# Kernel optimization log

Measured on AMD Instinct MI355X. Metric: run time of the kernel, lower is better.

The kernel has to match this reference:

```python
import jax, jax.numpy as jnp
import numpy as np
from jax import lax

B, S, H, E, TOP_K = 4, 2048, 8192, 256, 8

def setup_inputs() -> dict:
    key = jax.random.key(0)
    kx, kw = jax.random.split(key)
    x = jax.random.normal(kx, (B, S, H), dtype=jnp.float32)
    # Dense kernel init scale ~ 1/sqrt(H)
    W_router = jax.random.normal(kw, (H, E), dtype=jnp.float32) * (1.0 / np.sqrt(H))
    return {"x": x, "W_router": W_router}

def reference(x, W_router):
    # router_logits: [B, S, E]
    router_logits = jnp.einsum('bsh,he->bse', x, W_router)
    top_logits, top_indices = lax.top_k(router_logits, k=TOP_K)  # [B,S,K]
    routing_weights = jax.nn.softmax(top_logits, axis=-1)        # [B,S,K]
    return routing_weights, top_indices, router_logits
```

## Files before the change

### kernel.cpp

```cpp
#include <hip/hip_runtime.h>
#include <math.h>
#include <float.h>

typedef _Float16 half8 __attribute__((ext_vector_type(8)));
typedef float f32x4 __attribute__((ext_vector_type(4)));

namespace {
constexpr int kH = 8192, kE = 256, kTopK = 8, kTok = 8192;
constexpr int kIdxOff = kTok * kTopK;
constexpr int kLogitsOff = 2 * kTok * kTopK;
constexpr int kBM = 128, kBN = 128, kBK = 32;
constexpr int kPadH = 40;
constexpr int kCand = 16;
constexpr float kEps = 5e-5f;
constexpr float kInvScale = 1.0f / 262144.0f;
constexpr size_t kWtF   = (size_t)kE * kH;
constexpr size_t kWtlF  = kWtF + (size_t)kE * kH / 2;
constexpr size_t kPartF = kWtF + (size_t)kE * kH;
constexpr size_t kPartStride = (size_t)kTok * kE;
}

__global__ __launch_bounds__(1024)
void prep_w(const float* __restrict__ W, float* __restrict__ Wt,
            _Float16* __restrict__ Wth, _Float16* __restrict__ Wtl) {
    __shared__ float tile[32][33];
    const int k0 = blockIdx.x * 32, e0 = blockIdx.y * 32;
    const int tx = threadIdx.x, ty = threadIdx.y;
    tile[ty][tx] = W[(size_t)(k0 + ty) * kE + (e0 + tx)];
    __syncthreads();
    const float v = tile[tx][ty];
    const size_t o = (size_t)(e0 + ty) * kH + (k0 + tx);
    Wt[o] = v;
    const float vs = v * 256.0f;
    const _Float16 h = (_Float16)vs;
    Wth[o] = h;
    Wtl[o] = (_Float16)(vs - (float)h);
}

__global__ __launch_bounds__(256, 2)
void router_gemm_mfma(const float* __restrict__ x,
                      const _Float16* __restrict__ Wth,
                      const _Float16* __restrict__ Wtl,
                      float* __restrict__ p0, float* __restrict__ pws,
                      int kchunk)
{
    __shared__ _Float16 sxh[kBM][kPadH], sxl[kBM][kPadH];
    __shared__ _Float16 swh[kBN][kPadH], swl[kBN][kPadH];

    const int tid  = threadIdx.x;
    const int lane = tid & 63;
    const int w    = tid >> 6;
    const int wm   = w >> 1, wn = w & 1;
    const int t0   = blockIdx.x * kBM;
    const int e0   = blockIdx.y * kBN;
    const int kc   = blockIdx.z;
    const int kbase = kc * kchunk;
    const int nsteps = kchunk / kBK;

    f32x4 acc[4][4];
    #pragma unroll
    for (int m = 0; m < 4; ++m)
        #pragma unroll
        for (int n = 0; n < 4; ++n) {
            acc[m][n][0] = 0.f; acc[m][n][1] = 0.f;
            acc[m][n][2] = 0.f; acc[m][n][3] = 0.f;
        }

    const int srow = tid >> 1;
    const int scg  = (tid & 1) << 4;
    const float*    xp  = x   + (size_t)(t0 + srow) * kH + kbase + scg;
    const _Float16* whp = Wth + (size_t)(e0 + srow) * kH + kbase + scg;
    const _Float16* wlp = Wtl + (size_t)(e0 + srow) * kH + kbase + scg;

    float4 xv0, xv1, xv2, xv3;
    uint4  wh0, wh1, wl0, wl1;
    {
        xv0 = *reinterpret_cast<const float4*>(xp);
        xv1 = *reinterpret_cast<const float4*>(xp + 4);
        xv2 = *reinterpret_cast<const float4*>(xp + 8);
        xv3 = *reinterpret_cast<const float4*>(xp + 12);
        wh0 = *reinterpret_cast<const uint4*>(whp);
        wh1 = *reinterpret_cast<const uint4*>(whp + 8);
        wl0 = *reinterpret_cast<const uint4*>(wlp);
        wl1 = *reinterpret_cast<const uint4*>(wlp + 8);
    }

    const int fr = lane & 15;
    const int fk = (lane >> 4) << 3;

    for (int t = 0; t < nsteps; ++t) {
        float xf[16];
        xf[0]=xv0.x; xf[1]=xv0.y; xf[2]=xv0.z; xf[3]=xv0.w;
        xf[4]=xv1.x; xf[5]=xv1.y; xf[6]=xv1.z; xf[7]=xv1.w;
        xf[8]=xv2.x; xf[9]=xv2.y; xf[10]=xv2.z; xf[11]=xv2.w;
        xf[12]=xv3.x; xf[13]=xv3.y; xf[14]=xv3.z; xf[15]=xv3.w;
        half8 h0, h1, l0, l1;
        #pragma unroll
        for (int i = 0; i < 8; ++i) {
            const float sA = xf[i] * 1024.0f;
            const _Float16 hA = (_Float16)sA;
            h0[i] = hA; l0[i] = (_Float16)(sA - (float)hA);
            const float sB = xf[i + 8] * 1024.0f;
            const _Float16 hB = (_Float16)sB;
            h1[i] = hB; l1[i] = (_Float16)(sB - (float)hB);
        }
        *reinterpret_cast<half8*>(&sxh[srow][scg])     = h0;
        *reinterpret_cast<half8*>(&sxh[srow][scg + 8]) = h1;
        *reinterpret_cast<half8*>(&sxl[srow][scg])     = l0;
        *reinterpret_cast<half8*>(&sxl[srow][scg + 8]) = l1;
        *reinterpret_cast<uint4*>(&swh[srow][scg])     = wh0;
        *reinterpret_cast<uint4*>(&swh[srow][scg + 8]) = wh1;
        *reinterpret_cast<uint4*>(&swl[srow][scg])     = wl0;
        *reinterpret_cast<uint4*>(&swl[srow][scg + 8]) = wl1;
        __syncthreads();

        if (t + 1 < nsteps) {
            const size_t o = (size_t)(t + 1) * kBK;
            xv0 = *reinterpret_cast<const float4*>(xp + o);
            xv1 = *reinterpret_cast<const float4*>(xp + o + 4);
            xv2 = *reinterpret_cast<const float4*>(xp + o + 8);
            xv3 = *reinterpret_cast<const float4*>(xp + o + 12);
            wh0 = *reinterpret_cast<const uint4*>(whp + o);
            wh1 = *reinterpret_cast<const uint4*>(whp + o + 8);
            wl0 = *reinterpret_cast<const uint4*>(wlp + o);
            wl1 = *reinterpret_cast<const uint4*>(wlp + o + 8);
        }

        half8 ah[4], al[4];
        #pragma unroll
        for (int m = 0; m < 4; ++m) {
            ah[m] = *reinterpret_cast<const half8*>(&sxh[(wm << 6) + (m << 4) + fr][fk]);
            al[m] = *reinterpret_cast<const half8*>(&sxl[(wm << 6) + (m << 4) + fr][fk]);
        }
        #pragma unroll
        for (int n = 0; n < 4; ++n) {
            const half8 bh = *reinterpret_cast<const half8*>(&swh[(wn << 6) + (n << 4) + fr][fk]);
            const half8 bl = *reinterpret_cast<const half8*>(&swl[(wn << 6) + (n << 4) + fr][fk]);
            #pragma unroll
            for (int m = 0; m < 4; ++m) {
                acc[m][n] = __builtin_amdgcn_mfma_f32_16x16x32_f16(ah[m], bh, acc[m][n], 0, 0, 0);
                acc[m][n] = __builtin_amdgcn_mfma_f32_16x16x32_f16(ah[m], bl, acc[m][n], 0, 0, 0);
                acc[m][n] = __builtin_amdgcn_mfma_f32_16x16x32_f16(al[m], bh, acc[m][n], 0, 0, 0);
            }
        }
        __syncthreads();
    }

    float* dst = (kc == 0) ? p0 : (pws + (size_t)(kc - 1) * kPartStride);
    const int r0 = (lane >> 4) << 2;
    const int c0 = lane & 15;
    #pragma unroll
    for (int m = 0; m < 4; ++m)
        #pragma unroll
        for (int n = 0; n < 4; ++n) {
            const int col = e0 + (wn << 6) + (n << 4) + c0;
            #pragma unroll
            for (int r = 0; r < 4; ++r) {
                const int row = t0 + (wm << 6) + (m << 4) + r0 + r;
                dst[(size_t)row * kE + col] = acc[m][n][r] * kInvScale;
            }
        }
}

#define ARGMAX_ROUND(r)                                                        \
    {                                                                          \
        float bv = v0; int bi = (lane << 2);                                   \
        if (v1 > bv) { bv = v1; bi = (lane << 2) + 1; }                        \
        if (v2 > bv) { bv = v2; bi = (lane << 2) + 2; }                        \
        if (v3 > bv) { bv = v3; bi = (lane << 2) + 3; }                        \
        _Pragma("unroll")                                                      \
        for (int off = 32; off > 0; off >>= 1) {                               \
            const float ov = __shfl_xor(bv, off, 64);                          \
            const int   oi = __shfl_xor(bi, off, 64);                          \
            if (ov > bv || (ov == bv && oi < bi)) { bv = ov; bi = oi; }        \
        }                                                                      \
        if (lane == (r)) { myv = bv; myi = bi; }                               \
        if ((bi >> 2) == lane) {                                               \
            const int m = bi & 3;                                              \
            if      (m == 0) v0 = -FLT_MAX;                                    \
            else if (m == 1) v1 = -FLT_MAX;                                    \
            else if (m == 2) v2 = -FLT_MAX;                                    \
            else             v3 = -FLT_MAX;                                    \
        }                                                                      \
    }

__global__ __launch_bounds__(256)
void combine_select(const float* __restrict__ x, const float* __restrict__ Wt,
                    const float* __restrict__ pws, float* __restrict__ out,
                    int npart)
{
    const int lane = threadIdx.x & 63;
    const int w    = threadIdx.x >> 6;
    const int row  = blockIdx.x * 4 + w;
    float* logits = out + kLogitsOff;
    const size_t rb = (size_t)row * kE + (lane << 2);

    float4 s = *reinterpret_cast<const float4*>(logits + rb);
    for (int p = 0; p < npart; ++p) {
        const float4 q = *reinterpret_cast<const float4*>(pws + (size_t)p * kPartStride + rb);
        s.x += q.x; s.y += q.y; s.z += q.z; s.w += q.w;
    }
    *reinterpret_cast<float4*>(logits + rb) = s;

    float v0 = s.x, v1 = s.y, v2 = s.z, v3 = s.w;
    float myv = -FLT_MAX; int myi = -1;

    #pragma unroll
    for (int r = 0; r < 9; ++r) ARGMAX_ROUND(r)

    const float nv = __shfl_down(myv, 1, 64);
    const unsigned long long amb = __ballot(lane < 8 && (myv - nv) < kEps);

    if (amb == 0ull) {
        const float m = __shfl(myv, 0, 64);
        const float e = (lane < kTopK) ? expf(myv - m) : 0.f;
        float t = e;
        #pragma unroll
        for (int off = 1; off < 8; off <<= 1) t += __shfl_xor(t, off, 64);
        if (lane < kTopK) {
            out[(size_t)row * kTopK + lane]           = e / t;
            out[kIdxOff + (size_t)row * kTopK + lane] = (float)myi;
        }
    } else {
        #pragma unroll
        for (int r = 9; r < kCand; ++r) ARGMAX_ROUND(r)

        const float* xr = x + (size_t)row * kH;
        double dv = -1.0e300;
        #pragma unroll 1
        for (int cg = 0; cg < kCand; cg += 4) {
            const int i0 = __shfl(myi, cg + 0, 64);
            const int i1 = __shfl(myi, cg + 1, 64);
            const int i2 = __shfl(myi, cg + 2, 64);
            const int i3 = __shfl(myi, cg + 3, 64);
            const float* w0 = Wt + (size_t)i0 * kH;
            const float* w1 = Wt + (size_t)i1 * kH;
            const float* w2 = Wt + (size_t)i2 * kH;
            const float* w3 = Wt + (size_t)i3 * kH;
            double a0 = 0.0, a1 = 0.0, a2 = 0.0, a3 = 0.0;
            for (int k = (lane << 2); k < kH; k += 256) {
                const float4 xv = *reinterpret_cast<const float4*>(xr + k);
                const float4 q0 = *reinterpret_cast<const float4*>(w0 + k);
                const float4 q1 = *reinterpret_cast<const float4*>(w1 + k);
                const float4 q2 = *reinterpret_cast<const float4*>(w2 + k);
                const float4 q3 = *reinterpret_cast<const float4*>(w3 + k);
                a0 = fma((double)xv.x, (double)q0.x, a0);
                a1 = fma((double)xv.x, (double)q1.x, a1);
                a2 = fma((double)xv.x, (double)q2.x, a2);
                a3 = fma((double)xv.x, (double)q3.x, a3);
                a0 = fma((double)xv.y, (double)q0.y, a0);
                a1 = fma((double)xv.y, (double)q1.y, a1);
                a2 = fma((double)xv.y, (double)q2.y, a2);
                a3 = fma((double)xv.y, (double)q3.y, a3);
                a0 = fma((double)xv.z, (double)q0.z, a0);
                a1 = fma((double)xv.z, (double)q1.z, a1);
                a2 = fma((double)xv.z, (double)q2.z, a2);
                a3 = fma((double)xv.z, (double)q3.z, a3);
                a0 = fma((double)xv.w, (double)q0.w, a0);
                a1 = fma((double)xv.w, (double)q1.w, a1);
                a2 = fma((double)xv.w, (double)q2.w, a2);
                a3 = fma((double)xv.w, (double)q3.w, a3);
            }
            #pragma unroll
            for (int off = 32; off > 0; off >>= 1) {
                a0 += __shfl_xor(a0, off, 64);
                a1 += __shfl_xor(a1, off, 64);
                a2 += __shfl_xor(a2, off, 64);
                a3 += __shfl_xor(a3, off, 64);
            }
            if (lane == cg + 0) dv = a0;
            if (lane == cg + 1) dv = a1;
            if (lane == cg + 2) dv = a2;
            if (lane == cg + 3) dv = a3;
        }

        double cv = dv; int ci = myi;
        double mx = 0.0, ssum = 0.0, keepv = 0.0; int keepi = 0;
        #pragma unroll 1
        for (int r = 0; r < kTopK; ++r) {
            double bv = cv; int bi = ci;
            #pragma unroll
            for (int off = 32; off > 0; off >>= 1) {
                const double ov = __shfl_xor(bv, off, 64);
                const int    oi = __shfl_xor(bi, off, 64);
                if (ov > bv || (ov == bv && oi < bi)) { bv = ov; bi = oi; }
            }
            if (r == 0) mx = bv;
            ssum += exp(bv - mx);
            if (lane == r) { keepv = bv; keepi = bi; }
            if (ci == bi) cv = -1.0e300;
        }
        if (lane < kTopK) {
            out[(size_t)row * kTopK + lane]           = (float)(exp(keepv - mx) / ssum);
            out[kIdxOff + (size_t)row * kTopK + lane] = (float)keepi;
        }
    }
}

extern "C" void kernel_launch(void* const* d_in, const int* in_sizes, int n_in,
                              void* d_out, int out_size, void* d_ws, size_t ws_size,
                              hipStream_t stream) {
    const float* x  = (const float*)d_in[0];
    const float* Wr = (const float*)d_in[1];
    float* out = (float*)d_out;
    float* Wt  = (float*)d_ws;
    _Float16* Wth = (_Float16*)((float*)d_ws + kWtF);
    _Float16* Wtl = (_Float16*)((float*)d_ws + kWtlF);
    float* pws = (float*)d_ws + kPartF;
    (void)in_sizes; (void)n_in; (void)out_size;

    const size_t need4 = (kPartF + 3 * kPartStride) * sizeof(float);
    const int nkc = (ws_size >= need4) ? 4 : 2;
    const int kchunk = kH / nkc;

    hipLaunchKernelGGL(prep_w, dim3(kH / 32, kE / 32), dim3(32, 32), 0, stream,
                       Wr, Wt, Wth, Wtl);
    hipLaunchKernelGGL(router_gemm_mfma, dim3(kTok / kBM, kE / kBN, nkc), dim3(256),
                       0, stream, x, Wth, Wtl, out + kLogitsOff, pws, kchunk);
    hipLaunchKernelGGL(combine_select, dim3(kTok / 4), dim3(256), 0, stream,
                       x, Wt, pws, out, nkc - 1);
}
```

Baseline: 215.4 us.

## Load weight tiles directly into LDS with swizzled layout and raise split-K

Weight hi/lo fp16 tiles are now loaded with global_load_lds, going straight from global memory to LDS and skipping registers. The prep kernel writes them in an XOR-swizzled k order so the unpadded LDS tile avoids bank conflicts on MFMA operand reads. The split-K count rises from 4 to 8 when the workspace allows, adding parallelism at the cost of more partial buffers for the combine kernel to read and reduce. The direct LDS writes happen in the same iteration as the compute, with no double buffering, so load latency may still be exposed.

```diff
diff --git a/kernel.cpp b/kernel.cpp
--- a/kernel.cpp
+++ b/kernel.cpp
@@ -20,6 +20,16 @@
 constexpr size_t kPartStride = (size_t)kTok * kE;
 }
 
+__device__ __forceinline__ void gld16(const _Float16* g, _Float16* l) {
+    __builtin_amdgcn_global_load_lds(
+        (const __attribute__((address_space(1))) void*)g,
+        (__attribute__((address_space(3))) void*)l, 16, 0, 0);
+}
+
+__device__ __forceinline__ int kswz(int e, int k) {
+    return (k & ~31) | (((((k >> 3) & 3) ^ ((e >> 1) & 3))) << 3) | (k & 7);
+}
+
 __global__ __launch_bounds__(1024)
 void prep_w(const float* __restrict__ W, float* __restrict__ Wt,
             _Float16* __restrict__ Wth, _Float16* __restrict__ Wtl) {
@@ -29,12 +39,13 @@
     tile[ty][tx] = W[(size_t)(k0 + ty) * kE + (e0 + tx)];
     __syncthreads();
     const float v = tile[tx][ty];
-    const size_t o = (size_t)(e0 + ty) * kH + (k0 + tx);
-    Wt[o] = v;
+    const int e = e0 + ty, k = k0 + tx;
+    Wt[(size_t)e * kH + k] = v;
     const float vs = v * 256.0f;
     const _Float16 h = (_Float16)vs;
-    Wth[o] = h;
-    Wtl[o] = (_Float16)(vs - (float)h);
+    const size_t os = (size_t)e * kH + kswz(e, k);
+    Wth[os] = h;
+    Wtl[os] = (_Float16)(vs - (float)h);
 }
 
 __global__ __launch_bounds__(256, 2)
@@ -44,8 +55,10 @@
                       float* __restrict__ p0, float* __restrict__ pws,
                       int kchunk)
 {
-    __shared__ _Float16 sxh[kBM][kPadH], sxl[kBM][kPadH];
-    __shared__ _Float16 swh[kBN][kPadH], swl[kBN][kPadH];
+    __shared__ __align__(16) _Float16 sxh[kBM * kPadH];
+    __shared__ __align__(16) _Float16 sxl[kBM * kPadH];
+    __shared__ __align__(16) _Float16 swh[kBN * kBK];
+    __shared__ __align__(16) _Float16 swl[kBN * kBK];
 
     const int tid  = threadIdx.x;
     const int lane = tid & 63;
@@ -53,8 +66,7 @@
     const int wm   = w >> 1, wn = w & 1;
     const int t0   = blockIdx.x * kBM;
     const int e0   = blockIdx.y * kBN;
-    const int kc   = blockIdx.z;
-    const int kbase = kc * kchunk;
+    const int kbase = blockIdx.z * kchunk;
     const int nsteps = kchunk / kBK;
 
     f32x4 acc[4][4];
@@ -66,29 +78,35 @@
             acc[m][n][2] = 0.f; acc[m][n][3] = 0.f;
         }
 
+    const size_t wro0 = (size_t)(e0 + (w << 4) + (lane >> 2)) * kH
+                        + kbase + ((lane & 3) << 3);
+    const size_t wro1 = wro0 + (size_t)64 * kH;
+    _Float16* lwh0 = swh + (w << 9);
+    _Float16* lwh1 = swh + (w << 9) + 2048;
+    _Float16* lwl0 = swl + (w << 9);
+    _Float16* lwl1 = swl + (w << 9) + 2048;
+
     const int srow = tid >> 1;
     const int scg  = (tid & 1) << 4;
-    const float*    xp  = x   + (size_t)(t0 + srow) * kH + kbase + scg;
-    const _Float16* whp = Wth + (size_t)(e0 + srow) * kH + kbase + scg;
-    const _Float16* wlp = Wtl + (size_t)(e0 + srow) * kH + kbase + scg;
-
-    float4 xv0, xv1, xv2, xv3;
-    uint4  wh0, wh1, wl0, wl1;
-    {
-        xv0 = *reinterpret_cast<const float4*>(xp);
-        xv1 = *reinterpret_cast<const float4*>(xp + 4);
-        xv2 = *reinterpret_cast<const float4*>(xp + 8);
-        xv3 = *reinterpret_cast<const float4*>(xp + 12);
-        wh0 = *reinterpret_cast<const uint4*>(whp);
-        wh1 = *reinterpret_cast<const uint4*>(whp + 8);
-        wl0 = *reinterpret_cast<const uint4*>(wlp);
-        wl1 = *reinterpret_cast<const uint4*>(wlp + 8);
-    }
-
-    const int fr = lane & 15;
-    const int fk = (lane >> 4) << 3;
+    const float* xp = x + (size_t)(t0 + srow) * kH + kbase + scg;
+
+    float4 xv0 = *reinterpret_cast<const float4*>(xp);
+    float4 xv1 = *reinterpret_cast<const float4*>(xp + 4);
+    float4 xv2 = *reinterpret_cast<const float4*>(xp + 8);
+    float4 xv3 = *reinterpret_cast<const float4*>(xp + 12);
+
+    const int fr  = lane & 15;
+    const int q   = lane >> 4;
+    const int fkA = q << 3;
+    const int fkB = ((q ^ ((fr >> 1) & 3)) << 3);
 
     for (int t = 0; t < nsteps; ++t) {
+        const size_t ko = (size_t)t << 5;
+        gld16(Wth + wro0 + ko, lwh0);
+        gld16(Wth + wro1 + ko, lwh1);
+        gld16(Wtl + wro0 + ko, lwl0);
+        gld16(Wtl + wro1 + ko, lwl1);
+
         float xf[16];
         xf[0]=xv0.x; xf[1]=xv0.y; xf[2]=xv0.z; xf[3]=xv0.w;
         xf[4]=xv1.x; xf[5]=xv1.y; xf[6]=xv1.z; xf[7]=xv1.w;
@@ -104,38 +122,33 @@
             const _Float16 hB = (_Float16)sB;
             h1[i] = hB; l1[i] = (_Float16)(sB - (float)hB);
         }
-        *reinterpret_cast<half8*>(&sxh[srow][scg])     = h0;
-        *reinterpret_cast<half8*>(&sxh[srow][scg + 8]) = h1;
-        *reinterpret_cast<half8*>(&sxl[srow][scg])     = l0;
-        *reinterpret_cast<half8*>(&sxl[srow][scg + 8]) = l1;
-        *reinterpret_cast<uint4*>(&swh[srow][scg])     = wh0;
-        *reinterpret_cast<uint4*>(&swh[srow][scg + 8]) = wh1;
-        *reinterpret_cast<uint4*>(&swl[srow][scg])     = wl0;
-        *reinterpret_cast<uint4*>(&swl[srow][scg + 8]) = wl1;
+        *reinterpret_cast<half8*>(&sxh[srow * kPadH + scg])     = h0;
+        *reinterpret_cast<half8*>(&sxh[srow * kPadH + scg + 8]) = h1;
+        *reinterpret_cast<half8*>(&sxl[srow * kPadH + scg])     = l0;
+        *reinterpret_cast<half8*>(&sxl[srow * kPadH + scg + 8]) = l1;
+
         __syncthreads();
 
         if (t + 1 < nsteps) {
-            const size_t o = (size_t)(t + 1) * kBK;
-            xv0 = *reinterpret_cast<const float4*>(xp + o);
-            xv1 = *reinterpret_cast<const float4*>(xp + o + 4);
-            xv2 = *reinterpret_cast<const float4*>(xp + o + 8);
-            xv3 = *reinterpret_cast<const float4*>(xp + o + 12);
-            wh0 = *reinterpret_cast<const uint4*>(whp + o);
-            wh1 = *reinterpret_cast<const uint4*>(whp + o + 8);
-            wl0 = *reinterpret_cast<const uint4*>(wlp + o);
-            wl1 = *reinterpret_cast<const uint4*>(wlp + o + 8);
+            const float* nx = xp + ((size_t)(t + 1) << 5);
+            xv0 = *reinterpret_cast<const float4*>(nx);
+            xv1 = *reinterpret_cast<const float4*>(nx + 4);
+            xv2 = *reinterpret_cast<const float4*>(nx + 8);
+            xv3 = *reinterpret_cast<const float4*>(nx + 12);
         }
 
         half8 ah[4], al[4];
         #pragma unroll
         for (int m = 0; m < 4; ++m) {
-            ah[m] = *reinterpret_cast<const half8*>(&sxh[(wm << 6) + (m << 4) + fr][fk]);
-            al[m] = *reinterpret_cast<const half8*>(&sxl[(wm << 6) + (m << 4) + fr][fk]);
+            const int arow = (wm << 6) + (m << 4) + fr;
+            ah[m] = *reinterpret_cast<const half8*>(&sxh[arow * kPadH + fkA]);
+            al[m] = *reinterpret_cast<const half8*>(&sxl[arow * kPadH + fkA]);
         }
         #pragma unroll
         for (int n = 0; n < 4; ++n) {
-            const half8 bh = *reinterpret_cast<const half8*>(&swh[(wn << 6) + (n << 4) + fr][fk]);
-            const half8 bl = *reinterpret_cast<const half8*>(&swl[(wn << 6) + (n << 4) + fr][fk]);
+            const int brow = (wn << 6) + (n << 4) + fr;
+            const half8 bh = *reinterpret_cast<const half8*>(&swh[brow * kBK + fkB]);
+            const half8 bl = *reinterpret_cast<const half8*>(&swl[brow * kBK + fkB]);
             #pragma unroll
             for (int m = 0; m < 4; ++m) {
                 acc[m][n] = __builtin_amdgcn_mfma_f32_16x16x32_f16(ah[m], bh, acc[m][n], 0, 0, 0);
@@ -146,7 +159,7 @@
         __syncthreads();
     }
 
-    float* dst = (kc == 0) ? p0 : (pws + (size_t)(kc - 1) * kPartStride);
+    float* dst = (blockIdx.z == 0) ? p0 : (pws + (size_t)(blockIdx.z - 1) * kPartStride);
     const int r0 = (lane >> 4) << 2;
     const int c0 = lane & 15;
     #pragma unroll
@@ -309,8 +322,8 @@
     float* pws = (float*)d_ws + kPartF;
     (void)in_sizes; (void)n_in; (void)out_size;
 
-    const size_t need4 = (kPartF + 3 * kPartStride) * sizeof(float);
-    const int nkc = (ws_size >= need4) ? 4 : 2;
+    const size_t need8 = (kPartF + 7 * kPartStride) * sizeof(float);
+    const int nkc = (ws_size >= need8) ? 8 : 4;
     const int kchunk = kH / nkc;
 
     hipLaunchKernelGGL(prep_w, dim3(kH / 32, kE / 32), dim3(32, 32), 0, stream,
```

Result: slower. 247.6 us (+14.9%).
